# Kernel tuning notes

Measured on AMD Instinct MI355X. Metric: run time of the kernel, lower is better.

Reference implementation:

```python
import jax, jax.numpy as jnp
import numpy as np

N_NODES = 100000


def gcn_conv(x, src, dst, W, b, n_nodes):
    # PyG GCNConv: x' = D^{-1/2} (A + I) D^{-1/2} (x @ W) + b
    # src/dst already include self-loops.
    h = x @ W  # [N, out]
    deg = jax.ops.segment_sum(jnp.ones_like(src, dtype=x.dtype), dst,
                              num_segments=n_nodes)  # includes self-loops -> deg >= 1
    dinv = jax.lax.rsqrt(deg)
    norm = dinv[src] * dinv[dst]  # [E+N]
    msgs = h[src] * norm[:, None]  # [E+N, out]
    out = jax.ops.segment_sum(msgs, dst, num_segments=n_nodes)
    return out + b


def setup_inputs() -> dict:
    key = jax.random.key(0)
    k1, k2, k3, k4 = jax.random.split(key, 4)
    in_dim, hid_dim, out_dim = 64, 128, 64
    n_edges = 1_600_000
    x = jax.random.normal(k1, (N_NODES, in_dim), dtype=jnp.float32)
    edge_index = jax.random.randint(k2, (2, n_edges), 0, N_NODES, dtype=jnp.int64)
    # Glorot-ish init for weights
    W1 = jax.random.normal(k3, (in_dim, hid_dim), dtype=jnp.float32) * (1.0 / np.sqrt(in_dim))
    W2 = jax.random.normal(k4, (hid_dim, out_dim), dtype=jnp.float32) * (1.0 / np.sqrt(hid_dim))
    b1 = jnp.zeros((hid_dim,), dtype=jnp.float32)
    b2 = jnp.zeros((out_dim,), dtype=jnp.float32)
    return {"x": x, "edge_index": edge_index, "W1": W1, "b1": b1, "W2": W2, "b2": b2}


def reference(x, edge_index, W1, b1, W2, b2):
    n = x.shape[0]
    loops = jnp.arange(n, dtype=edge_index.dtype)
    src = jnp.concatenate([edge_index[0], loops])
    dst = jnp.concatenate([edge_index[1], loops])
    h = gcn_conv(x, src, dst, W1, b1, n)
    h = jax.nn.relu(h)
    out = gcn_conv(h, src, dst, W2, b2, n)
    return out
```

## Files before the change

kernel.cpp:

```cpp
#include <hip/hip_runtime.h>
#include <hip/hip_fp16.h>


#define DIM 64
#define NB 256
#define SPAN 391
#define BK_TILE 4096
#define BK_PER 16

__device__ __forceinline__ void atomAddF(float* p, float v) {
    unsafeAtomicAdd(p, v);
}

__device__ __forceinline__ void h8_add(const float4 v, float* acc) {
    const __half2* hp = (const __half2*)&v;
    #pragma unroll
    for (int i = 0; i < 4; ++i) {
        float2 t = __half22float2(hp[i]);
        acc[2 * i] += t.x;
        acc[2 * i + 1] += t.y;
    }
}
__device__ __forceinline__ float4 f8_to_h8(const float* f) {
    __half2 hh[4];
    hh[0] = __float22half2_rn(make_float2(f[0], f[1]));
    hh[1] = __float22half2_rn(make_float2(f[2], f[3]));
    hh[2] = __float22half2_rn(make_float2(f[4], f[5]));
    hh[3] = __float22half2_rn(make_float2(f[6], f[7]));
    return *(float4*)hh;
}

__global__ __launch_bounds__(256) void k_zero256(int* p) {
    p[threadIdx.x] = 0;
}
__global__ __launch_bounds__(256) void k_hist256(const int* __restrict__ ei,
                                                 int* __restrict__ bucketCnt, int E) {
    __shared__ int h[NB];
    const int tid = threadIdx.x;
    h[tid] = 0;
    __syncthreads();
    const int base = blockIdx.x * BK_TILE;
    #pragma unroll
    for (int j = 0; j < BK_TILE; j += 256) {
        int e = base + j + tid;
        if (e < E) atomicAdd(&h[(unsigned)ei[E + e] / (unsigned)SPAN], 1);
    }
    __syncthreads();
    if (h[tid]) atomicAdd(&bucketCnt[tid], h[tid]);
}
__global__ __launch_bounds__(256) void k_scan_b(const int* __restrict__ bucketCnt,
                                                int* __restrict__ bucketBase,
                                                int* __restrict__ gcur) {
    __shared__ int s[NB];
    const int tid = threadIdx.x;
    int v = bucketCnt[tid];
    s[tid] = v;
    __syncthreads();
    for (int off = 1; off < NB; off <<= 1) {
        int t = (tid >= off) ? s[tid - off] : 0;
        __syncthreads();
        s[tid] += t;
        __syncthreads();
    }
    int ex = s[tid] - v;
    bucketBase[tid] = ex;
    gcur[tid] = ex;
    if (tid == NB - 1) bucketBase[NB] = s[NB - 1];
}

__global__ __launch_bounds__(256) void k_bucket(const int* __restrict__ ei,
                                                int* __restrict__ gcur,
                                                unsigned* __restrict__ pairs, int E) {
    __shared__ int scn[NB];
    __shared__ int run[NB];
    __shared__ int lbase[NB];
    __shared__ int gbase[NB];
    __shared__ unsigned stage[BK_TILE];
    __shared__ unsigned char bkt[BK_TILE];
    const int tid = threadIdx.x;
    const int base = blockIdx.x * BK_TILE;

    scn[tid] = 0;
    __syncthreads();

    unsigned pv[BK_PER];
    int bv[BK_PER];
    #pragma unroll
    for (int j = 0; j < BK_PER; ++j) {
        int e = base + j * 256 + tid;
        if (e < E) {
            unsigned s = (unsigned)ei[e];
            unsigned d = (unsigned)ei[E + e];
            int b = (int)(d / (unsigned)SPAN);
            bv[j] = b;
            pv[j] = (s << 9) | (d - (unsigned)b * SPAN);
            atomicAdd(&scn[b], 1);
        } else bv[j] = -1;
    }
    __syncthreads();
    int c = scn[tid];
    for (int off = 1; off < 256; off <<= 1) {
        int t = (tid >= off) ? scn[tid - off] : 0;
        __syncthreads();
        scn[tid] += t;
        __syncthreads();
    }
    int ex = scn[tid] - c;
    lbase[tid] = ex;
    run[tid] = ex;
    if (c > 0) gbase[tid] = atomicAdd(&gcur[tid], c);
    __syncthreads();

    #pragma unroll
    for (int j = 0; j < BK_PER; ++j) {
        if (bv[j] >= 0) {
            int p = atomicAdd(&run[bv[j]], 1);
            stage[p] = pv[j];
            bkt[p] = (unsigned char)bv[j];
        }
    }
    __syncthreads();

    int total = min(BK_TILE, E - base);
    for (int i = tid; i < total; i += 256) {
        int bb = bkt[i];
        pairs[gbase[bb] + (i - lbase[bb])] = stage[i];
    }
}

__global__ __launch_bounds__(256) void k_finish(const unsigned* __restrict__ pairs,
                                                const int* __restrict__ bucketBase,
                                                int* __restrict__ row_ptr,
                                                float* __restrict__ dinv,
                                                int* __restrict__ col, int N) {
    __shared__ int lh[512];
    __shared__ int sa[512];
    __shared__ int sb[512];
    __shared__ int lcur[SPAN];
    const int tid = threadIdx.x;
    const int b = blockIdx.x;
    const int lo = b * SPAN;
    const int hi = min(lo + SPAN, N);
    const int nn = hi - lo;
    const int p0 = bucketBase[b];
    const int p1 = bucketBase[b + 1];

    for (int i = tid; i < 512; i += 256) lh[i] = 0;
    __syncthreads();
    for (int e = p0 + tid; e < p1; e += 256)
        atomicAdd(&lh[pairs[e] & 511u], 1);
    __syncthreads();
    int* cur = sa;
    int* nxt = sb;
    for (int i = tid; i < 512; i += 256) sa[i] = lh[i];
    __syncthreads();
    for (int off = 1; off < 512; off <<= 1) {
        for (int i = tid; i < 512; i += 256)
            nxt[i] = cur[i] + ((i >= off) ? cur[i - off] : 0);
        __syncthreads();
        int* t = cur; cur = nxt; nxt = t;
    }
    for (int i = tid; i < nn; i += 256) {
        int cnt  = lh[i];
        int base = p0 + cur[i] - cnt;
        row_ptr[lo + i] = base;
        lcur[i] = base;
        dinv[lo + i] = rsqrtf(1.0f + (float)cnt);
    }
    if (b == NB - 1 && tid == 0) row_ptr[N] = p1;
    __syncthreads();
    for (int e = p0 + tid; e < p1; e += 256) {
        unsigned pr = pairs[e];
        int pos = atomicAdd(&lcur[pr & 511u], 1);
        col[pos] = (int)(pr >> 9);
    }
}

__global__ __launch_bounds__(256) void k_prescale_h(const float* __restrict__ x,
                                                    const float* __restrict__ dinv,
                                                    __half* __restrict__ Y, int n) {
    int g = blockIdx.x * 256 + threadIdx.x;
    int i = g >> 3, seg = g & 7;
    if (i >= n) return;
    float di = dinv[i];
    float4 a = ((const float4*)x)[(long)i * 16 + seg * 2];
    float4 b = ((const float4*)x)[(long)i * 16 + seg * 2 + 1];
    float f[8] = {a.x * di, a.y * di, a.z * di, a.w * di,
                  b.x * di, b.y * di, b.z * di, b.w * di};
    ((float4*)Y)[(long)i * 8 + seg] = f8_to_h8(f);
}

template<bool BIAS, bool OUT_HALF>
__global__ __launch_bounds__(256) void k_agg_h(const int* __restrict__ row_ptr,
                                               const int* __restrict__ col,
                                               const float* __restrict__ dinv,
                                               const __half* __restrict__ ph,
                                               const float* __restrict__ bias,
                                               void* __restrict__ outv, int n) {
    int g = blockIdx.x * 32 + (threadIdx.x >> 3);
    if (g >= n) return;
    int lane = threadIdx.x & 7;
    const float4* h4 = (const float4*)ph;
    float accA[8] = {}, accB[8] = {};
    h8_add(h4[(long)g * 8 + lane], accA);
    int e = row_ptr[g], e1 = row_ptr[g + 1];
    for (; e + 8 <= e1; e += 8) {
        int s0 = col[e], s1 = col[e + 1], s2 = col[e + 2], s3 = col[e + 3];
        int s4 = col[e + 4], s5 = col[e + 5], s6 = col[e + 6], s7 = col[e + 7];
        float4 v0 = h4[(long)s0 * 8 + lane];
        float4 v1 = h4[(long)s1 * 8 + lane];
        float4 v2 = h4[(long)s2 * 8 + lane];
        float4 v3 = h4[(long)s3 * 8 + lane];
        float4 v4 = h4[(long)s4 * 8 + lane];
        float4 v5 = h4[(long)s5 * 8 + lane];
        float4 v6 = h4[(long)s6 * 8 + lane];
        float4 v7 = h4[(long)s7 * 8 + lane];
        h8_add(v0, accA); h8_add(v1, accB);
        h8_add(v2, accA); h8_add(v3, accB);
        h8_add(v4, accA); h8_add(v5, accB);
        h8_add(v6, accA); h8_add(v7, accB);
    }
    for (; e + 2 <= e1; e += 2) {
        float4 v0 = h4[(long)col[e] * 8 + lane];
        float4 v1 = h4[(long)col[e + 1] * 8 + lane];
        h8_add(v0, accA); h8_add(v1, accB);
    }
    if (e < e1) h8_add(h4[(long)col[e] * 8 + lane], accA);

    float di = dinv[g];
    float r[8];
    #pragma unroll
    for (int i = 0; i < 8; ++i) r[i] = (accA[i] + accB[i]) * di;
    if (OUT_HALF) {
        ((float4*)outv)[(long)g * 8 + lane] = f8_to_h8(r);
    } else {
        if (BIAS) {
            float4 b0 = ((const float4*)bias)[lane * 2];
            float4 b1 = ((const float4*)bias)[lane * 2 + 1];
            r[0] += b0.x; r[1] += b0.y; r[2] += b0.z; r[3] += b0.w;
            r[4] += b1.x; r[5] += b1.y; r[6] += b1.z; r[7] += b1.w;
        }
        ((float4*)outv)[(long)g * 16 + lane * 2]     = make_float4(r[0], r[1], r[2], r[3]);
        ((float4*)outv)[(long)g * 16 + lane * 2 + 1] = make_float4(r[4], r[5], r[6], r[7]);
    }
}

__global__ __launch_bounds__(256) void k_mlp_h(const __half* __restrict__ G,
                                               const float* __restrict__ W1,
                                               const float* __restrict__ b1,
                                               const float* __restrict__ W2,
                                               const float* __restrict__ dscale,
                                               __half* __restrict__ T,
                                               int M) {
    __shared__ float Ws[64 * 128];
    __shared__ float HA[64 * 132];
    const int tid = threadIdx.x;
    const int row0 = blockIdx.x * 64;
    const int ty = tid >> 4;
    const int tx = tid & 15;

    #pragma unroll
    for (int l = 0; l < 2; ++l) {
        int idx = l * 256 + tid;
        int r = idx >> 3, seg = idx & 7;
        int gr = row0 + r;
        float4 raw = make_float4(0.f, 0.f, 0.f, 0.f);
        if (gr < M) raw = ((const float4*)G)[(long)gr * 8 + seg];
        float f[8] = {};
        h8_add(raw, f);
        *(float4*)&HA[r * 68 + seg * 8]     = make_float4(f[0], f[1], f[2], f[3]);
        *(float4*)&HA[r * 68 + seg * 8 + 4] = make_float4(f[4], f[5], f[6], f[7]);
    }
    #pragma unroll
    for (int l = 0; l < 8; ++l) {
        int idx = (l * 256 + tid) * 4;
        *(float4*)&Ws[idx] = *(const float4*)&W1[idx];
    }
    __syncthreads();

    float4 accA[4], accB[4];
    #pragma unroll
    for (int i = 0; i < 4; ++i) {
        accA[i] = make_float4(0.f, 0.f, 0.f, 0.f);
        accB[i] = make_float4(0.f, 0.f, 0.f, 0.f);
    }
    for (int k4 = 0; k4 < 64; k4 += 4) {
        float4 a[4];
        #pragma unroll
        for (int i = 0; i < 4; ++i) a[i] = *(const float4*)&HA[(ty * 4 + i) * 68 + k4];
        #pragma unroll
        for (int kk = 0; kk < 4; ++kk) {
            const float* wr = &Ws[(k4 + kk) * 128 + tx * 8];
            float4 wA = *(const float4*)wr;
            float4 wB = *(const float4*)(wr + 4);
            #pragma unroll
            for (int i = 0; i < 4; ++i) {
                float ak = (&a[i].x)[kk];
                accA[i].x += ak * wA.x; accA[i].y += ak * wA.y;
                accA[i].z += ak * wA.z; accA[i].w += ak * wA.w;
                accB[i].x += ak * wB.x; accB[i].y += ak * wB.y;
                accB[i].z += ak * wB.z; accB[i].w += ak * wB.w;
            }
        }
    }
    __syncthreads();

    {
        float4 bA = *(const float4*)&b1[tx * 8];
        float4 bB = *(const float4*)&b1[tx * 8 + 4];
        #pragma unroll
        for (int i = 0; i < 4; ++i) {
            float4 hA = make_float4(fmaxf(accA[i].x + bA.x, 0.f), fmaxf(accA[i].y + bA.y, 0.f),
                                    fmaxf(accA[i].z + bA.z, 0.f), fmaxf(accA[i].w + bA.w, 0.f));
            float4 hB = make_float4(fmaxf(accB[i].x + bB.x, 0.f), fmaxf(accB[i].y + bB.y, 0.f),
                                    fmaxf(accB[i].z + bB.z, 0.f), fmaxf(accB[i].w + bB.w, 0.f));
            *(float4*)&HA[(ty * 4 + i) * 132 + tx * 8 + 0] = hA;
            *(float4*)&HA[(ty * 4 + i) * 132 + tx * 8 + 4] = hB;
        }
    }
    #pragma unroll
    for (int l = 0; l < 8; ++l) {
        int idx = (l * 256 + tid) * 4;
        *(float4*)&Ws[idx] = *(const float4*)&W2[idx];
    }
    __syncthreads();

    float4 o[4];
    #pragma unroll
    for (int i = 0; i < 4; ++i) o[i] = make_float4(0.f, 0.f, 0.f, 0.f);
    for (int k4 = 0; k4 < 128; k4 += 4) {
        float4 a[4];
        #pragma unroll
        for (int i = 0; i < 4; ++i) a[i] = *(const float4*)&HA[(ty * 4 + i) * 132 + k4];
        #pragma unroll
        for (int kk = 0; kk < 4; ++kk) {
            float4 w = *(const float4*)&Ws[(k4 + kk) * 64 + tx * 4];
            #pragma unroll
            for (int i = 0; i < 4; ++i) {
                float ak = (&a[i].x)[kk];
                o[i].x += ak * w.x; o[i].y += ak * w.y;
                o[i].z += ak * w.z; o[i].w += ak * w.w;
            }
        }
    }
    #pragma unroll
    for (int i = 0; i < 4; ++i) {
        int gr = row0 + ty * 4 + i;
        if (gr < M) {
            float sc = dscale[gr];
            __half2 p0 = __float22half2_rn(make_float2(o[i].x * sc, o[i].y * sc));
            __half2 p1 = __float22half2_rn(make_float2(o[i].z * sc, o[i].w * sc));
            float2 st;
            ((__half2*)&st)[0] = p0;
            ((__half2*)&st)[1] = p1;
            *(float2*)(T + (long)gr * 64 + tx * 4) = st;
        }
    }
}

__global__ __launch_bounds__(256) void k_init_deg(float* deg, int n) {
    int i = blockIdx.x * 256 + threadIdx.x;
    if (i < n) deg[i] = 1.0f;
}
__global__ __launch_bounds__(256) void k_count_deg(const int* __restrict__ ei, float* deg, int E) {
    int e = blockIdx.x * 256 + threadIdx.x;
    if (e < E) atomAddF(&deg[ei[E + e]], 1.0f);
}
__global__ __launch_bounds__(256) void k_rsqrt(float* deg, int n) {
    int i = blockIdx.x * 256 + threadIdx.x;
    if (i < n) deg[i] = rsqrtf(deg[i]);
}
template<bool BIAS>
__global__ __launch_bounds__(256) void k_self(const float* __restrict__ src,
                                              const float* __restrict__ dinv,
                                              const float* __restrict__ b,
                                              float* __restrict__ out, int n) {
    int g = blockIdx.x * 256 + threadIdx.x;
    int i = g >> 4, c = g & 15;
    if (i >= n) return;
    float di = dinv[i];
    float s = di * di;
    float4 v = *(const float4*)&src[(long)i * DIM + c * 4];
    float4 r = make_float4(v.x * s, v.y * s, v.z * s, v.w * s);
    if (BIAS) {
        float4 bv = *(const float4*)&b[c * 4];
        r.x += bv.x; r.y += bv.y; r.z += bv.z; r.w += bv.w;
    }
    *(float4*)&out[(long)i * DIM + c * 4] = r;
}
__global__ __launch_bounds__(256) void k_edge_agg(const int* __restrict__ ei,
                                                  const float* __restrict__ dinv,
                                                  const float* __restrict__ h,
                                                  float* __restrict__ out, int E) {
    int t = threadIdx.x;
    int e = blockIdx.x * 16 + (t >> 4);
    if (e >= E) return;
    int lane = t & 15;
    int s = ei[e];
    int d = ei[E + e];
    float norm = dinv[s] * dinv[d];
    float4 hv = *(const float4*)&h[(long)s * DIM + lane * 4];
    float* o = &out[(long)d * DIM + lane * 4];
    atomAddF(o + 0, hv.x * norm);
    atomAddF(o + 1, hv.y * norm);
    atomAddF(o + 2, hv.z * norm);
    atomAddF(o + 3, hv.w * norm);
}
__global__ __launch_bounds__(256) void k_mlp_f(const float* __restrict__ G,
                                               const float* __restrict__ W1,
                                               const float* __restrict__ b1,
                                               const float* __restrict__ W2,
                                               float* __restrict__ T, int M) {
    __shared__ float Ws[64 * 128];
    __shared__ float HA[64 * 132];
    const int tid = threadIdx.x;
    const int row0 = blockIdx.x * 64;
    const int ty = tid >> 4;
    const int tx = tid & 15;
    #pragma unroll
    for (int l = 0; l < 4; ++l) {
        int idx = l * 256 + tid;
        int r = idx >> 4, cv = idx & 15;
        int gr = row0 + r;
        float4 v = make_float4(0.f, 0.f, 0.f, 0.f);
        if (gr < M) v = *(const float4*)&G[(long)gr * DIM + cv * 4];
        *(float4*)&HA[r * 68 + cv * 4] = v;
    }
    #pragma unroll
    for (int l = 0; l < 8; ++l) {
        int idx = (l * 256 + tid) * 4;
        *(float4*)&Ws[idx] = *(const float4*)&W1[idx];
    }
    __syncthreads();
    float4 accA[4], accB[4];
    #pragma unroll
    for (int i = 0; i < 4; ++i) {
        accA[i] = make_float4(0.f, 0.f, 0.f, 0.f);
        accB[i] = make_float4(0.f, 0.f, 0.f, 0.f);
    }
    for (int k4 = 0; k4 < 64; k4 += 4) {
        float4 a[4];
        #pragma unroll
        for (int i = 0; i < 4; ++i) a[i] = *(const float4*)&HA[(ty * 4 + i) * 68 + k4];
        #pragma unroll
        for (int kk = 0; kk < 4; ++kk) {
            const float* wr = &Ws[(k4 + kk) * 128 + tx * 8];
            float4 wA = *(const float4*)wr;
            float4 wB = *(const float4*)(wr + 4);
            #pragma unroll
            for (int i = 0; i < 4; ++i) {
                float ak = (&a[i].x)[kk];
                accA[i].x += ak * wA.x; accA[i].y += ak * wA.y;
                accA[i].z += ak * wA.z; accA[i].w += ak * wA.w;
                accB[i].x += ak * wB.x; accB[i].y += ak * wB.y;
                accB[i].z += ak * wB.z; accB[i].w += ak * wB.w;
            }
        }
    }
    __syncthreads();
    {
        float4 bA = *(const float4*)&b1[tx * 8];
        float4 bB = *(const float4*)&b1[tx * 8 + 4];
        #pragma unroll
        for (int i = 0; i < 4; ++i) {
            float4 hA = make_float4(fmaxf(accA[i].x + bA.x, 0.f), fmaxf(accA[i].y + bA.y, 0.f),
                                    fmaxf(accA[i].z + bA.z, 0.f), fmaxf(accA[i].w + bA.w, 0.f));
            float4 hB = make_float4(fmaxf(accB[i].x + bB.x, 0.f), fmaxf(accB[i].y + bB.y, 0.f),
                                    fmaxf(accB[i].z + bB.z, 0.f), fmaxf(accB[i].w + bB.w, 0.f));
            *(float4*)&HA[(ty * 4 + i) * 132 + tx * 8 + 0] = hA;
            *(float4*)&HA[(ty * 4 + i) * 132 + tx * 8 + 4] = hB;
        }
    }
    #pragma unroll
    for (int l = 0; l < 8; ++l) {
        int idx = (l * 256 + tid) * 4;
        *(float4*)&Ws[idx] = *(const float4*)&W2[idx];
    }
    __syncthreads();
    float4 o[4];
    #pragma unroll
    for (int i = 0; i < 4; ++i) o[i] = make_float4(0.f, 0.f, 0.f, 0.f);
    for (int k4 = 0; k4 < 128; k4 += 4) {
        float4 a[4];
        #pragma unroll
        for (int i = 0; i < 4; ++i) a[i] = *(const float4*)&HA[(ty * 4 + i) * 132 + k4];
        #pragma unroll
        for (int kk = 0; kk < 4; ++kk) {
            float4 w = *(const float4*)&Ws[(k4 + kk) * 64 + tx * 4];
            #pragma unroll
            for (int i = 0; i < 4; ++i) {
                float ak = (&a[i].x)[kk];
                o[i].x += ak * w.x; o[i].y += ak * w.y;
                o[i].z += ak * w.z; o[i].w += ak * w.w;
            }
        }
    }
    #pragma unroll
    for (int i = 0; i < 4; ++i) {
        int gr = row0 + ty * 4 + i;
        if (gr < M) *(float4*)&T[(long)gr * DIM + tx * 4] = o[i];
    }
}

extern "C" void kernel_launch(void* const* d_in, const int* in_sizes, int n_in,
                              void* d_out, int out_size, void* d_ws, size_t ws_size,
                              hipStream_t stream) {
    const float* x  = (const float*)d_in[0];
    const int*   ei = (const int*)d_in[1];
    const float* W1 = (const float*)d_in[2];
    const float* b1 = (const float*)d_in[3];
    const float* W2 = (const float*)d_in[4];
    const float* b2 = (const float*)d_in[5];
    float* out = (float*)d_out;

    const int N = in_sizes[0] / DIM;
    const int E = in_sizes[1] / 2;

    const int gn   = (N + 255) / 256;
    const int ge   = (E + 255) / 256;
    const int gagg = (N + 31) / 32;
    const int gmlp = (N + 63) / 64;
    const int grow8 = ((long)N * 8 + 255) / 256;
    const int gbk  = (E + BK_TILE - 1) / BK_TILE;

    size_t off = 0;
    auto bump = [&](size_t bytes) { size_t o = off; off = (off + bytes + 255) & ~(size_t)255; return o; };
    size_t o_dinv   = bump((size_t)N * 4);
    size_t o_rowptr = bump((size_t)(N + 1) * 4);
    size_t o_bcnt   = bump(NB * 4);
    size_t o_bbase  = bump((NB + 1) * 4);
    size_t o_gcur   = bump(NB * 4);
    size_t o_col    = bump((size_t)E * 4);
    size_t o_X      = bump((size_t)N * DIM * 2);
    size_t o_Y      = bump((size_t)N * DIM * 2);
    size_t need_csr = off;

    char* ws = (char*)d_ws;

    if (ws_size >= need_csr) {
        float*    dinv   = (float*)(ws + o_dinv);
        int*      rowptr = (int*)(ws + o_rowptr);
        int*      bcnt   = (int*)(ws + o_bcnt);
        int*      bbase  = (int*)(ws + o_bbase);
        int*      gcur   = (int*)(ws + o_gcur);
        int*      col    = (int*)(ws + o_col);
        __half*   X      = (__half*)(ws + o_X);
        __half*   Y      = (__half*)(ws + o_Y);
        unsigned* pairs  = (unsigned*)(ws + o_Y);

        k_zero256<<<1, 256, 0, stream>>>(bcnt);
        k_hist256<<<gbk, 256, 0, stream>>>(ei, bcnt, E);
        k_scan_b<<<1, 256, 0, stream>>>(bcnt, bbase, gcur);
        k_bucket<<<gbk, 256, 0, stream>>>(ei, gcur, pairs, E);
        k_finish<<<NB, 256, 0, stream>>>(pairs, bbase, rowptr, dinv, col, N);

        k_prescale_h<<<grow8, 256, 0, stream>>>(x, dinv, Y, N);
        k_agg_h<false, true><<<gagg, 256, 0, stream>>>(rowptr, col, dinv, Y, nullptr, X, N);
        k_mlp_h<<<gmlp, 256, 0, stream>>>(X, W1, b1, W2, dinv, X, N);
        k_agg_h<true, false><<<gagg, 256, 0, stream>>>(rowptr, col, dinv, X, b2, out, N);
    } else {
        float* dinv = (float*)ws;
        float* buf  = (float*)(ws + 512 * 1024);
        int grow16 = ((long)N * 16 + 255) / 256;
        int gedge = (E + 15) / 16;

        k_init_deg<<<gn, 256, 0, stream>>>(dinv, N);
        k_count_deg<<<ge, 256, 0, stream>>>(ei, dinv, E);
        k_rsqrt<<<gn, 256, 0, stream>>>(dinv, N);

        k_self<false><<<grow16, 256, 0, stream>>>(x, dinv, nullptr, buf, N);
        k_edge_agg<<<gedge, 256, 0, stream>>>(ei, dinv, x, buf, E);
        k_mlp_f<<<gmlp, 256, 0, stream>>>(buf, W1, b1, W2, buf, N);
        k_self<true><<<grow16, 256, 0, stream>>>(buf, dinv, b2, out, N);
        k_edge_agg<<<gedge, 256, 0, stream>>>(ei, dinv, buf, out, E);
    }
}
```

Measured before the change: 257.2 us.

## Replace scalar FP32 fused MLP with FP16 MFMA kernel and pre-transposed weights

The fused two-layer dense transform now runs on matrix cores via 16x16x32 FP16 MFMA instead of FP32 FMA loops over shared-memory tiles. A small new kernel converts and transposes W1 and W2 to FP16 in workspace each call so B fragments load directly from global memory. The hidden activations are kept as FP16 in LDS between the two GEMMs and outputs are staged through LDS for coalesced stores. This trades some precision (FP16 weights and hidden layer) and adds one extra launch in exchange for much cheaper dense compute.

```diff
diff --git a/kernel.cpp b/kernel.cpp
--- a/kernel.cpp
+++ b/kernel.cpp
@@ -7,6 +7,9 @@
 #define SPAN 391
 #define BK_TILE 4096
 #define BK_PER 16
+
+typedef _Float16 f16x8 __attribute__((ext_vector_type(8)));
+typedef float f32x4 __attribute__((ext_vector_type(4)));
 
 __device__ __forceinline__ void atomAddF(float* p, float v) {
     unsafeAtomicAdd(p, v);
@@ -245,115 +248,101 @@
     }
 }
 
-__global__ __launch_bounds__(256) void k_mlp_h(const __half* __restrict__ G,
-                                               const float* __restrict__ W1,
-                                               const float* __restrict__ b1,
+__global__ __launch_bounds__(256) void k_wconv(const float* __restrict__ W1,
                                                const float* __restrict__ W2,
-                                               const float* __restrict__ dscale,
-                                               __half* __restrict__ T,
-                                               int M) {
-    __shared__ float Ws[64 * 128];
-    __shared__ float HA[64 * 132];
+                                               _Float16* __restrict__ W1t,
+                                               _Float16* __restrict__ W2t) {
+    int idx = blockIdx.x * 256 + threadIdx.x;
+    if (idx < 8192) {
+        int n = idx >> 6, k = idx & 63;
+        W1t[idx] = (_Float16)W1[k * 128 + n];
+    } else if (idx < 16384) {
+        int j = idx - 8192;
+        int n = j >> 7, k = j & 127;
+        W2t[j] = (_Float16)W2[k * 64 + n];
+    }
+}
+
+__global__ __launch_bounds__(256) void k_mlp_mfma(const _Float16* __restrict__ G,
+                                                  const _Float16* __restrict__ W1t,
+                                                  const float* __restrict__ b1,
+                                                  const _Float16* __restrict__ W2t,
+                                                  const float* __restrict__ dscale,
+                                                  _Float16* __restrict__ T,
+                                                  int M) {
+    __shared__ _Float16 Hs[64 * 136];
+    __shared__ _Float16 Os[64 * 72];
     const int tid = threadIdx.x;
     const int row0 = blockIdx.x * 64;
-    const int ty = tid >> 4;
-    const int tx = tid & 15;
-
-    #pragma unroll
-    for (int l = 0; l < 2; ++l) {
-        int idx = l * 256 + tid;
-        int r = idx >> 3, seg = idx & 7;
+    const int wv = tid >> 6;
+    const int lane = tid & 63;
+    const int lr = lane & 15;
+    const int lg = lane >> 4;
+
+    const int arow = row0 + wv * 16 + lr;
+    f16x8 a0 = {}, a1 = {};
+    if (arow < M) {
+        a0 = *(const f16x8*)(G + (long)arow * 64 + lg * 8);
+        a1 = *(const f16x8*)(G + (long)arow * 64 + 32 + lg * 8);
+    }
+    const _Float16* wb1 = W1t + lr * 64 + lg * 8;
+    f32x4 acc[8];
+    #pragma unroll
+    for (int nt = 0; nt < 8; ++nt) acc[nt] = (f32x4){0.f, 0.f, 0.f, 0.f};
+    #pragma unroll
+    for (int nt = 0; nt < 8; ++nt) {
+        f16x8 b0 = *(const f16x8*)(wb1 + nt * 1024);
+        f16x8 bK = *(const f16x8*)(wb1 + nt * 1024 + 32);
+        acc[nt] = __builtin_amdgcn_mfma_f32_16x16x32_f16(a0, b0, acc[nt], 0, 0, 0);
+        acc[nt] = __builtin_amdgcn_mfma_f32_16x16x32_f16(a1, bK, acc[nt], 0, 0, 0);
+    }
+    #pragma unroll
+    for (int nt = 0; nt < 8; ++nt) {
+        float bv = b1[nt * 16 + lr];
+        #pragma unroll
+        for (int r = 0; r < 4; ++r) {
+            float h = fmaxf(acc[nt][r] + bv, 0.f);
+            Hs[(wv * 16 + lg * 4 + r) * 136 + nt * 16 + lr] = (_Float16)h;
+        }
+    }
+    __syncthreads();
+
+    const _Float16* wb2 = W2t + lr * 128 + lg * 8;
+    const _Float16* hrow = Hs + (wv * 16 + lr) * 136 + lg * 8;
+    f32x4 acc2[4];
+    #pragma unroll
+    for (int nt = 0; nt < 4; ++nt) acc2[nt] = (f32x4){0.f, 0.f, 0.f, 0.f};
+    #pragma unroll
+    for (int kk = 0; kk < 4; ++kk) {
+        f16x8 a = *(const f16x8*)(hrow + kk * 32);
+        #pragma unroll
+        for (int nt = 0; nt < 4; ++nt) {
+            f16x8 b = *(const f16x8*)(wb2 + nt * 2048 + kk * 32);
+            acc2[nt] = __builtin_amdgcn_mfma_f32_16x16x32_f16(a, b, acc2[nt], 0, 0, 0);
+        }
+    }
+    float sc[4];
+    #pragma unroll
+    for (int r = 0; r < 4; ++r) {
+        int gr = row0 + wv * 16 + lg * 4 + r;
+        sc[r] = (gr < M) ? dscale[gr] : 0.f;
+    }
+    #pragma unroll
+    for (int nt = 0; nt < 4; ++nt) {
+        #pragma unroll
+        for (int r = 0; r < 4; ++r)
+            Os[(wv * 16 + lg * 4 + r) * 72 + nt * 16 + lr] = (_Float16)(acc2[nt][r] * sc[r]);
+    }
+    __syncthreads();
+
+    {
+        int r = tid >> 2, c0 = (tid & 3) * 16;
         int gr = row0 + r;
-        float4 raw = make_float4(0.f, 0.f, 0.f, 0.f);
-        if (gr < M) raw = ((const float4*)G)[(long)gr * 8 + seg];
-        float f[8] = {};
-        h8_add(raw, f);
-        *(float4*)&HA[r * 68 + seg * 8]     = make_float4(f[0], f[1], f[2], f[3]);
-        *(float4*)&HA[r * 68 + seg * 8 + 4] = make_float4(f[4], f[5], f[6], f[7]);
-    }
-    #pragma unroll
-    for (int l = 0; l < 8; ++l) {
-        int idx = (l * 256 + tid) * 4;
-        *(float4*)&Ws[idx] = *(const float4*)&W1[idx];
-    }
-    __syncthreads();
-
-    float4 accA[4], accB[4];
-    #pragma unroll
-    for (int i = 0; i < 4; ++i) {
-        accA[i] = make_float4(0.f, 0.f, 0.f, 0.f);
-        accB[i] = make_float4(0.f, 0.f, 0.f, 0.f);
-    }
-    for (int k4 = 0; k4 < 64; k4 += 4) {
-        float4 a[4];
-        #pragma unroll
-        for (int i = 0; i < 4; ++i) a[i] = *(const float4*)&HA[(ty * 4 + i) * 68 + k4];
-        #pragma unroll
-        for (int kk = 0; kk < 4; ++kk) {
-            const float* wr = &Ws[(k4 + kk) * 128 + tx * 8];
-            float4 wA = *(const float4*)wr;
-            float4 wB = *(const float4*)(wr + 4);
-            #pragma unroll
-            for (int i = 0; i < 4; ++i) {
-                float ak = (&a[i].x)[kk];
-                accA[i].x += ak * wA.x; accA[i].y += ak * wA.y;
-                accA[i].z += ak * wA.z; accA[i].w += ak * wA.w;
-                accB[i].x += ak * wB.x; accB[i].y += ak * wB.y;
-                accB[i].z += ak * wB.z; accB[i].w += ak * wB.w;
-            }
-        }
-    }
-    __syncthreads();
-
-    {
-        float4 bA = *(const float4*)&b1[tx * 8];
-        float4 bB = *(const float4*)&b1[tx * 8 + 4];
-        #pragma unroll
-        for (int i = 0; i < 4; ++i) {
-            float4 hA = make_float4(fmaxf(accA[i].x + bA.x, 0.f), fmaxf(accA[i].y + bA.y, 0.f),
-                                    fmaxf(accA[i].z + bA.z, 0.f), fmaxf(accA[i].w + bA.w, 0.f));
-            float4 hB = make_float4(fmaxf(accB[i].x + bB.x, 0.f), fmaxf(accB[i].y + bB.y, 0.f),
-                                    fmaxf(accB[i].z + bB.z, 0.f), fmaxf(accB[i].w + bB.w, 0.f));
-            *(float4*)&HA[(ty * 4 + i) * 132 + tx * 8 + 0] = hA;
-            *(float4*)&HA[(ty * 4 + i) * 132 + tx * 8 + 4] = hB;
-        }
-    }
-    #pragma unroll
-    for (int l = 0; l < 8; ++l) {
-        int idx = (l * 256 + tid) * 4;
-        *(float4*)&Ws[idx] = *(const float4*)&W2[idx];
-    }
-    __syncthreads();
-
-    float4 o[4];
-    #pragma unroll
-    for (int i = 0; i < 4; ++i) o[i] = make_float4(0.f, 0.f, 0.f, 0.f);
-    for (int k4 = 0; k4 < 128; k4 += 4) {
-        float4 a[4];
-        #pragma unroll
-        for (int i = 0; i < 4; ++i) a[i] = *(const float4*)&HA[(ty * 4 + i) * 132 + k4];
-        #pragma unroll
-        for (int kk = 0; kk < 4; ++kk) {
-            float4 w = *(const float4*)&Ws[(k4 + kk) * 64 + tx * 4];
-            #pragma unroll
-            for (int i = 0; i < 4; ++i) {
-                float ak = (&a[i].x)[kk];
-                o[i].x += ak * w.x; o[i].y += ak * w.y;
-                o[i].z += ak * w.z; o[i].w += ak * w.w;
-            }
-        }
-    }
-    #pragma unroll
-    for (int i = 0; i < 4; ++i) {
-        int gr = row0 + ty * 4 + i;
         if (gr < M) {
-            float sc = dscale[gr];
-            __half2 p0 = __float22half2_rn(make_float2(o[i].x * sc, o[i].y * sc));
-            __half2 p1 = __float22half2_rn(make_float2(o[i].z * sc, o[i].w * sc));
-            float2 st;
-            ((__half2*)&st)[0] = p0;
-            ((__half2*)&st)[1] = p1;
-            *(float2*)(T + (long)gr * 64 + tx * 4) = st;
+            f16x8 v0 = *(const f16x8*)(Os + r * 72 + c0);
+            f16x8 v1 = *(const f16x8*)(Os + r * 72 + c0 + 8);
+            *(f16x8*)(T + (long)gr * 64 + c0) = v0;
+            *(f16x8*)(T + (long)gr * 64 + c0 + 8) = v1;
         }
     }
 }
@@ -533,6 +522,8 @@
     size_t o_col    = bump((size_t)E * 4);
     size_t o_X      = bump((size_t)N * DIM * 2);
     size_t o_Y      = bump((size_t)N * DIM * 2);
+    size_t o_W1t    = bump(128 * 64 * 2);
+    size_t o_W2t    = bump(64 * 128 * 2);
     size_t need_csr = off;
 
     char* ws = (char*)d_ws;
@@ -547,7 +538,10 @@
         __half*   X      = (__half*)(ws + o_X);
         __half*   Y      = (__half*)(ws + o_Y);
         unsigned* pairs  = (unsigned*)(ws + o_Y);
-
+        _Float16* W1t    = (_Float16*)(ws + o_W1t);
+        _Float16* W2t    = (_Float16*)(ws + o_W2t);
+
+        k_wconv<<<64, 256, 0, stream>>>(W1, W2, W1t, W2t);
         k_zero256<<<1, 256, 0, stream>>>(bcnt);
         k_hist256<<<gbk, 256, 0, stream>>>(ei, bcnt, E);
         k_scan_b<<<1, 256, 0, stream>>>(bcnt, bbase, gcur);
@@ -556,7 +550,8 @@
 
         k_prescale_h<<<grow8, 256, 0, stream>>>(x, dinv, Y, N);
         k_agg_h<false, true><<<gagg, 256, 0, stream>>>(rowptr, col, dinv, Y, nullptr, X, N);
-        k_mlp_h<<<gmlp, 256, 0, stream>>>(X, W1, b1, W2, dinv, X, N);
+        k_mlp_mfma<<<gmlp, 256, 0, stream>>>((const _Float16*)X, W1t, b1, W2t, dinv,
+                                             (_Float16*)X, N);
         k_agg_h<true, false><<<gagg, 256, 0, stream>>>(rowptr, col, dinv, X, b2, out, N);
     } else {
         float* dinv = (float*)ws;
```

New measurement: 239.1 us. 1.08x faster.
